# Performance work log

Measured on AMD Instinct MI355X. Metric: run time of the kernel, lower is better.

Reference implementation:

```python
import jax, jax.numpy as jnp
import numpy as np
import math

N = 8192
DIM = 256

def setup_inputs() -> dict:
    key = jax.random.key(0)
    k1, k2, k3 = jax.random.split(key, 3)
    h = jax.random.normal(k1, (N, DIM), dtype=jnp.float32)
    # xavier_uniform with gain=1.414 for square [dim, dim] matrices
    gain = 1.414
    bound = gain * math.sqrt(6.0 / (DIM + DIM))
    Wq = jax.random.uniform(k2, (DIM, DIM), dtype=jnp.float32, minval=-bound, maxval=bound)
    Wk = jax.random.uniform(k3, (DIM, DIM), dtype=jnp.float32, minval=-bound, maxval=bound)
    return {"h": h, "Wq": Wq, "Wk": Wk}

def reference(h, Wq, Wk):
    dim = h.shape[1]
    q = h @ Wq                                   # [N, dim]
    k = h @ Wk                                   # [N, dim]
    e = (q @ k.T) / jnp.sqrt(jnp.asarray(dim, h.dtype))  # [N, N]
    attention = jax.nn.softmax(e, axis=1)        # row-wise softmax
    attention = attention.mean(axis=0)           # [N], column-mean over rows
    x = attention @ h                            # [dim]
    return x
```

## Files before the change

### kernel.cpp

```cpp
#include <hip/hip_runtime.h>
#include <cstdint>
#include <cstddef>


#define N_ROWS 8192
#define DIM    256

typedef __bf16 bf16x8 __attribute__((ext_vector_type(8)));
typedef unsigned short u16x8 __attribute__((ext_vector_type(8)));
typedef float f32x16 __attribute__((ext_vector_type(16)));

__device__ __forceinline__ uint16_t f2bf(float f) {
    uint32_t u = __float_as_uint(f);
    uint32_t r = (u + 0x7fffu + ((u >> 16) & 1u)) >> 16;
    return (uint16_t)r;
}

__global__ __launch_bounds__(256) void proj_kernel(
        const float* __restrict__ h, const float* __restrict__ Wq,
        const float* __restrict__ Wk, uint16_t* __restrict__ qf,
        uint16_t* __restrict__ kf, float* __restrict__ l_arr,
        float* __restrict__ c_arr, float* __restrict__ out) {
    __shared__ alignas(16) uint16_t wb[256 * 128];
    __shared__ alignas(16) uint16_t rep[4][2048];
    const int tid = threadIdx.x, lane = tid & 63, wave = tid >> 6;
    const int which = blockIdx.x & 1;
    const int rt = blockIdx.x >> 1;

    if (blockIdx.x < 32)       l_arr[blockIdx.x * 256 + tid] = 0.0f;
    else if (blockIdx.x < 64)  c_arr[(blockIdx.x - 32) * 256 + tid] = 0.0f;
    else if (blockIdx.x == 64) out[tid] = 0.0f;

    const float* __restrict__ W = which ? Wk : Wq;
    uint16_t* __restrict__ dst = which ? kf : qf;
    const float scale = which ? 1.0f : 0.0625f;

    bf16x8 afrag[16];
    {
        const int r = rt * 32 + (lane & 31);
        const float* hp = h + (size_t)r * DIM + ((lane >> 5) * 8);
#pragma unroll
        for (int a0 = 0; a0 < 16; a0++) {
            float4 f0 = *(const float4*)(hp + a0 * 16);
            float4 f1 = *(const float4*)(hp + a0 * 16 + 4);
            u16x8 f;
            f[0] = f2bf(f0.x); f[1] = f2bf(f0.y); f[2] = f2bf(f0.z); f[3] = f2bf(f0.w);
            f[4] = f2bf(f1.x); f[5] = f2bf(f1.y); f[6] = f2bf(f1.z); f[7] = f2bf(f1.w);
            afrag[a0] = __builtin_bit_cast(bf16x8, f);
        }
    }

    for (int p = 0; p < 2; p++) {
        __syncthreads();
#pragma unroll
        for (int c = 0; c < 32; c++) {
            int f = c * 256 + tid;
            int k = f >> 5, nc = (f & 31) * 4;
            float4 w4 = *(const float4*)&W[(size_t)k * DIM + p * 128 + nc];
            ushort4 b;
            b.x = f2bf(w4.x); b.y = f2bf(w4.y); b.z = f2bf(w4.z); b.w = f2bf(w4.w);
            *(ushort4*)&wb[k * 128 + nc] = b;
        }
        __syncthreads();

        f32x16 acc;
#pragma unroll
        for (int i = 0; i < 16; i++) acc[i] = 0.0f;
        const int cl = wave * 32 + (lane & 31);
#pragma unroll
        for (int a0 = 0; a0 < 16; a0++) {
            const int kb = a0 * 16 + (lane >> 5) * 8;
            u16x8 f;
#pragma unroll
            for (int j = 0; j < 8; j++) f[j] = wb[(kb + j) * 128 + cl];
            acc = __builtin_amdgcn_mfma_f32_32x32x16_bf16(
                afrag[a0], __builtin_bit_cast(bf16x8, f), acc, 0, 0, 0);
        }

        {
            const int dcl = lane & 31;
            const int a0o = dcl >> 4, hi = (dcl >> 3) & 1, j = dcl & 7;
            const int ilb = 4 * (lane >> 5);
#pragma unroll
            for (int reg = 0; reg < 16; reg++) {
                int il = ilb + (reg & 3) + 8 * (reg >> 2);
                rep[wave][(size_t)((a0o * 64) + il + 32 * hi) * 8 + j] =
                    f2bf(acc[reg] * scale);
            }
            const uint4* rp = (const uint4*)&rep[wave][0];
            uint4* gp = (uint4*)(dst + (size_t)rt * 8192 +
                                 (size_t)(p * 8 + wave * 2) * 512);
            gp[lane * 2]     = rp[lane * 2];
            gp[lane * 2 + 1] = rp[lane * 2 + 1];
        }
    }
}

template <int MODE>
__global__ __launch_bounds__(256, 2) void qk_pass(
        const uint16_t* __restrict__ qf, const uint16_t* __restrict__ kf,
        float* __restrict__ l_arr, float* __restrict__ c_arr) {
    __shared__ float c_lds[512];
    const int tid = threadIdx.x, lane = tid & 63, wave = tid >> 6;
    const int bid = blockIdx.x;
    const int cc = ((bid & 7) << 1) | ((bid >> 3) & 1);
    const int rb = bid >> 4;
    const int t0 = rb * 8 + wave * 2;

    const uint4* qp = (const uint4*)qf;
    bf16x8 q0[16], q1[16];
#pragma unroll
    for (int a0 = 0; a0 < 16; a0++) {
        q0[a0] = __builtin_bit_cast(bf16x8, qp[(size_t)t0 * 1024 + a0 * 64 + lane]);
        q1[a0] = __builtin_bit_cast(bf16x8, qp[(size_t)(t0 + 1) * 1024 + a0 * 64 + lane]);
    }

    float rs0[16], rs1[16];
    float rr0[16], rr1[16];
    if (MODE == 0) {
#pragma unroll
        for (int r = 0; r < 16; r++) { rs0[r] = 0.0f; rs1[r] = 0.0f; }
    } else {
#pragma unroll
        for (int r = 0; r < 16; r++) {
            int ro = (r & 3) + 8 * (r >> 2) + 4 * (lane >> 5);
            rr0[r] = 1.0f / (8192.0f * l_arr[t0 * 32 + ro]);
            rr1[r] = 1.0f / (8192.0f * l_arr[(t0 + 1) * 32 + ro]);
        }
        for (int i = tid; i < 512; i += 256) c_lds[i] = 0.0f;
        __syncthreads();
    }

    const uint4* kp = (const uint4*)kf;
    bf16x8 b[2][4];
    {
        const uint4* kt = kp + (size_t)(cc * 16) * 1024;
#pragma unroll
        for (int i = 0; i < 4; i++)
            b[0][i] = __builtin_bit_cast(bf16x8, kt[i * 64 + lane]);
    }

    f32x16 acc0, acc1;
#pragma unroll
    for (int i = 0; i < 16; i++) { acc0[i] = 0.0f; acc1[i] = 0.0f; }

    for (int s = 0; s < 16; s++) {
        const uint4* kt  = kp + (size_t)(cc * 16 + s) * 1024;
        const uint4* ktn = kt + 1024;
#pragma unroll
        for (int qd = 0; qd < 4; qd++) {
            const int cur = qd & 1, nxt = cur ^ 1;
            if (qd < 3) {
#pragma unroll
                for (int i = 0; i < 4; i++)
                    b[nxt][i] = __builtin_bit_cast(bf16x8,
                        kt[((qd + 1) * 4 + i) * 64 + lane]);
            } else if (s < 15) {
#pragma unroll
                for (int i = 0; i < 4; i++)
                    b[nxt][i] = __builtin_bit_cast(bf16x8, ktn[i * 64 + lane]);
            }
#pragma unroll
            for (int i = 0; i < 4; i++) {
                acc0 = __builtin_amdgcn_mfma_f32_32x32x16_bf16(
                    q0[qd * 4 + i], b[cur][i], acc0, 0, 0, 0);
                acc1 = __builtin_amdgcn_mfma_f32_32x32x16_bf16(
                    q1[qd * 4 + i], b[cur][i], acc1, 0, 0, 0);
            }
        }
        if (MODE == 0) {
#pragma unroll
            for (int r = 0; r < 16; r++) {
                rs0[r] += __expf(acc0[r]);  acc0[r] = 0.0f;
                rs1[r] += __expf(acc1[r]);  acc1[r] = 0.0f;
            }
        } else {
            float sv = 0.0f;
#pragma unroll
            for (int r = 0; r < 16; r++) {
                sv += __expf(acc0[r]) * rr0[r];  acc0[r] = 0.0f;
                sv += __expf(acc1[r]) * rr1[r];  acc1[r] = 0.0f;
            }
            sv += __shfl_xor(sv, 32);
            if (lane < 32) atomicAdd(&c_lds[s * 32 + lane], sv);
        }
    }

    if (MODE == 0) {
#pragma unroll
        for (int r = 0; r < 16; r++) {
            int ro = (r & 3) + 8 * (r >> 2) + 4 * (lane >> 5);
            float v0 = rs0[r], v1 = rs1[r];
            v0 += __shfl_xor(v0, 1);  v0 += __shfl_xor(v0, 2);
            v0 += __shfl_xor(v0, 4);  v0 += __shfl_xor(v0, 8);
            v0 += __shfl_xor(v0, 16);
            v1 += __shfl_xor(v1, 1);  v1 += __shfl_xor(v1, 2);
            v1 += __shfl_xor(v1, 4);  v1 += __shfl_xor(v1, 8);
            v1 += __shfl_xor(v1, 16);
            if ((lane & 31) == 0) {
                atomicAdd(&l_arr[t0 * 32 + ro], v0);
                atomicAdd(&l_arr[(t0 + 1) * 32 + ro], v1);
            }
        }
    } else {
        __syncthreads();
        for (int i = tid; i < 512; i += 256) atomicAdd(&c_arr[cc * 512 + i], c_lds[i]);
    }
}

__global__ __launch_bounds__(256) void finish_kernel(
        const float* __restrict__ h, const float* __restrict__ c_arr,
        float* __restrict__ out) {
    const int d = threadIdx.x;
    const int j0 = blockIdx.x * 64;
    float acc = 0.0f;
    for (int j = j0; j < j0 + 64; j++) acc += c_arr[j] * h[(size_t)j * DIM + d];
    atomicAdd(&out[d], acc);
}

extern "C" void kernel_launch(void* const* d_in, const int* in_sizes, int n_in,
                              void* d_out, int out_size, void* d_ws, size_t ws_size,
                              hipStream_t stream) {
    const float* h  = (const float*)d_in[0];
    const float* Wq = (const float*)d_in[1];
    const float* Wk = (const float*)d_in[2];

    uint16_t* qf = (uint16_t*)d_ws;
    uint16_t* kf = qf + (size_t)N_ROWS * DIM;
    float* l_arr = (float*)((char*)d_ws + (size_t)8 * 1024 * 1024);
    float* c_arr = l_arr + N_ROWS;
    float* out = (float*)d_out;

    proj_kernel<<<512, 256, 0, stream>>>(h, Wq, Wk, qf, kf, l_arr, c_arr, out);
    qk_pass<0><<<512, 256, 0, stream>>>(qf, kf, l_arr, c_arr);
    qk_pass<1><<<512, 256, 0, stream>>>(qf, kf, l_arr, c_arr);
    finish_kernel<<<128, 256, 0, stream>>>(h, c_arr, out);
}
```

Before: 182.1 us.

## Retile QK passes per XCD, split accumulators, use exp2, stage h via LDS

The QK passes are retiled so each wave handles one 32-row Q tile across 32 K column tiles, with block-to-XCD mapping chosen for L2 locality. Two interleaved MFMA accumulators break the dependency chain. The log2(e) factor is folded into the Q scale so the native exp2 can be used. Occupancy hint rises to 3 blocks per CU, and the projection kernel now stages h through LDS, reusing the weight buffer for output repacking. The trade-off is reloading K tiles per single Q tile, which halves K reuse per MFMA compared with the previous two-tile scheme.

```diff
diff --git a/kernel.cpp b/kernel.cpp
--- a/kernel.cpp
+++ b/kernel.cpp
@@ -14,6 +14,14 @@
     uint32_t u = __float_as_uint(f);
     uint32_t r = (u + 0x7fffu + ((u >> 16) & 1u)) >> 16;
     return (uint16_t)r;
+}
+
+__device__ __forceinline__ float fexp2(float x) {
+#if __has_builtin(__builtin_amdgcn_exp2f)
+    return __builtin_amdgcn_exp2f(x);
+#else
+    return __expf(x * 0.69314718056f);
+#endif
 }
 
 __global__ __launch_bounds__(256) void proj_kernel(
@@ -22,7 +30,6 @@
         uint16_t* __restrict__ kf, float* __restrict__ l_arr,
         float* __restrict__ c_arr, float* __restrict__ out) {
     __shared__ alignas(16) uint16_t wb[256 * 128];
-    __shared__ alignas(16) uint16_t rep[4][2048];
     const int tid = threadIdx.x, lane = tid & 63, wave = tid >> 6;
     const int which = blockIdx.x & 1;
     const int rt = blockIdx.x >> 1;
@@ -33,16 +40,27 @@
 
     const float* __restrict__ W = which ? Wk : Wq;
     uint16_t* __restrict__ dst = which ? kf : qf;
-    const float scale = which ? 1.0f : 0.0625f;
+    const float scale = which ? 1.0f : (0.0625f * 1.44269504089f);
+
+    {
+        float* hb = (float*)wb;
+        for (int i = tid; i < 2048; i += 256) {
+            int r = i >> 6, c = (i & 63) * 4;
+            float4 v = *(const float4*)&h[(size_t)(rt * 32 + r) * DIM + c];
+            *(float4*)&hb[r * 260 + c] = v;
+        }
+    }
+    __syncthreads();
 
     bf16x8 afrag[16];
     {
-        const int r = rt * 32 + (lane & 31);
-        const float* hp = h + (size_t)r * DIM + ((lane >> 5) * 8);
+        const float* hb = (const float*)wb;
+        const int r = lane & 31;
 #pragma unroll
         for (int a0 = 0; a0 < 16; a0++) {
-            float4 f0 = *(const float4*)(hp + a0 * 16);
-            float4 f1 = *(const float4*)(hp + a0 * 16 + 4);
+            const int c0 = a0 * 16 + (lane >> 5) * 8;
+            float4 f0 = *(const float4*)&hb[r * 260 + c0];
+            float4 f1 = *(const float4*)&hb[r * 260 + c0 + 4];
             u16x8 f;
             f[0] = f2bf(f0.x); f[1] = f2bf(f0.y); f[2] = f2bf(f0.z); f[3] = f2bf(f0.w);
             f[4] = f2bf(f1.x); f[5] = f2bf(f1.y); f[6] = f2bf(f1.z); f[7] = f2bf(f1.w);
@@ -76,76 +94,78 @@
             acc = __builtin_amdgcn_mfma_f32_32x32x16_bf16(
                 afrag[a0], __builtin_bit_cast(bf16x8, f), acc, 0, 0, 0);
         }
+        __syncthreads();
 
         {
+            uint16_t* rp = &wb[wave * 2048];
             const int dcl = lane & 31;
             const int a0o = dcl >> 4, hi = (dcl >> 3) & 1, j = dcl & 7;
             const int ilb = 4 * (lane >> 5);
 #pragma unroll
             for (int reg = 0; reg < 16; reg++) {
                 int il = ilb + (reg & 3) + 8 * (reg >> 2);
-                rep[wave][(size_t)((a0o * 64) + il + 32 * hi) * 8 + j] =
+                rp[(size_t)((a0o * 64) + il + 32 * hi) * 8 + j] =
                     f2bf(acc[reg] * scale);
             }
-            const uint4* rp = (const uint4*)&rep[wave][0];
+            const uint4* rv = (const uint4*)rp;
             uint4* gp = (uint4*)(dst + (size_t)rt * 8192 +
                                  (size_t)(p * 8 + wave * 2) * 512);
-            gp[lane * 2]     = rp[lane * 2];
-            gp[lane * 2 + 1] = rp[lane * 2 + 1];
+            gp[lane * 2]     = rv[lane * 2];
+            gp[lane * 2 + 1] = rv[lane * 2 + 1];
         }
     }
 }
 
 template <int MODE>
-__global__ __launch_bounds__(256, 2) void qk_pass(
+__global__ __launch_bounds__(256, 3) void qk_pass(
         const uint16_t* __restrict__ qf, const uint16_t* __restrict__ kf,
         float* __restrict__ l_arr, float* __restrict__ c_arr) {
-    __shared__ float c_lds[512];
+    __shared__ float c_lds[1024];
     const int tid = threadIdx.x, lane = tid & 63, wave = tid >> 6;
     const int bid = blockIdx.x;
-    const int cc = ((bid & 7) << 1) | ((bid >> 3) & 1);
-    const int rb = bid >> 4;
-    const int t0 = rb * 8 + wave * 2;
+    const int xcd = bid & 7, w = bid >> 3;
+    const int xr = xcd >> 1, xc = xcd & 1;
+    const int rw = w & 15, cw = w >> 4;
+    const int t0  = xr * 64 + rw * 4 + wave;
+    const int ct0 = xc * 128 + cw * 32;
+    const int row0 = t0 * 32;
 
     const uint4* qp = (const uint4*)qf;
-    bf16x8 q0[16], q1[16];
-#pragma unroll
-    for (int a0 = 0; a0 < 16; a0++) {
-        q0[a0] = __builtin_bit_cast(bf16x8, qp[(size_t)t0 * 1024 + a0 * 64 + lane]);
-        q1[a0] = __builtin_bit_cast(bf16x8, qp[(size_t)(t0 + 1) * 1024 + a0 * 64 + lane]);
-    }
-
-    float rs0[16], rs1[16];
-    float rr0[16], rr1[16];
+    bf16x8 q[16];
+#pragma unroll
+    for (int a0 = 0; a0 < 16; a0++)
+        q[a0] = __builtin_bit_cast(bf16x8, qp[(size_t)t0 * 1024 + a0 * 64 + lane]);
+
+    float rs[16];
+    float rr[16];
     if (MODE == 0) {
 #pragma unroll
-        for (int r = 0; r < 16; r++) { rs0[r] = 0.0f; rs1[r] = 0.0f; }
+        for (int r = 0; r < 16; r++) rs[r] = 0.0f;
     } else {
 #pragma unroll
         for (int r = 0; r < 16; r++) {
             int ro = (r & 3) + 8 * (r >> 2) + 4 * (lane >> 5);
-            rr0[r] = 1.0f / (8192.0f * l_arr[t0 * 32 + ro]);
-            rr1[r] = 1.0f / (8192.0f * l_arr[(t0 + 1) * 32 + ro]);
-        }
-        for (int i = tid; i < 512; i += 256) c_lds[i] = 0.0f;
+            rr[r] = 1.0f / (8192.0f * l_arr[row0 + ro]);
+        }
+        for (int i = tid; i < 1024; i += 256) c_lds[i] = 0.0f;
         __syncthreads();
     }
 
     const uint4* kp = (const uint4*)kf;
     bf16x8 b[2][4];
     {
-        const uint4* kt = kp + (size_t)(cc * 16) * 1024;
+        const uint4* kt = kp + (size_t)ct0 * 1024;
 #pragma unroll
         for (int i = 0; i < 4; i++)
             b[0][i] = __builtin_bit_cast(bf16x8, kt[i * 64 + lane]);
     }
 
-    f32x16 acc0, acc1;
-#pragma unroll
-    for (int i = 0; i < 16; i++) { acc0[i] = 0.0f; acc1[i] = 0.0f; }
-
-    for (int s = 0; s < 16; s++) {
-        const uint4* kt  = kp + (size_t)(cc * 16 + s) * 1024;
+    f32x16 ae, ao;
+#pragma unroll
+    for (int i = 0; i < 16; i++) { ae[i] = 0.0f; ao[i] = 0.0f; }
+
+    for (int t = 0; t < 32; t++) {
+        const uint4* kt  = kp + (size_t)(ct0 + t) * 1024;
         const uint4* ktn = kt + 1024;
 #pragma unroll
         for (int qd = 0; qd < 4; qd++) {
@@ -155,56 +175,49 @@
                 for (int i = 0; i < 4; i++)
                     b[nxt][i] = __builtin_bit_cast(bf16x8,
                         kt[((qd + 1) * 4 + i) * 64 + lane]);
-            } else if (s < 15) {
+            } else if (t < 31) {
 #pragma unroll
                 for (int i = 0; i < 4; i++)
                     b[nxt][i] = __builtin_bit_cast(bf16x8, ktn[i * 64 + lane]);
             }
-#pragma unroll
-            for (int i = 0; i < 4; i++) {
-                acc0 = __builtin_amdgcn_mfma_f32_32x32x16_bf16(
-                    q0[qd * 4 + i], b[cur][i], acc0, 0, 0, 0);
-                acc1 = __builtin_amdgcn_mfma_f32_32x32x16_bf16(
-                    q1[qd * 4 + i], b[cur][i], acc1, 0, 0, 0);
-            }
+            ae = __builtin_amdgcn_mfma_f32_32x32x16_bf16(q[qd * 4 + 0], b[cur][0], ae, 0, 0, 0);
+            ao = __builtin_amdgcn_mfma_f32_32x32x16_bf16(q[qd * 4 + 1], b[cur][1], ao, 0, 0, 0);
+            ae = __builtin_amdgcn_mfma_f32_32x32x16_bf16(q[qd * 4 + 2], b[cur][2], ae, 0, 0, 0);
+            ao = __builtin_amdgcn_mfma_f32_32x32x16_bf16(q[qd * 4 + 3], b[cur][3], ao, 0, 0, 0);
         }
         if (MODE == 0) {
 #pragma unroll
             for (int r = 0; r < 16; r++) {
-                rs0[r] += __expf(acc0[r]);  acc0[r] = 0.0f;
-                rs1[r] += __expf(acc1[r]);  acc1[r] = 0.0f;
+                rs[r] += fexp2(ae[r] + ao[r]);
+                ae[r] = 0.0f;  ao[r] = 0.0f;
             }
         } else {
             float sv = 0.0f;
 #pragma unroll
             for (int r = 0; r < 16; r++) {
-                sv += __expf(acc0[r]) * rr0[r];  acc0[r] = 0.0f;
-                sv += __expf(acc1[r]) * rr1[r];  acc1[r] = 0.0f;
+                sv += fexp2(ae[r] + ao[r]) * rr[r];
+                ae[r] = 0.0f;  ao[r] = 0.0f;
             }
             sv += __shfl_xor(sv, 32);
-            if (lane < 32) atomicAdd(&c_lds[s * 32 + lane], sv);
+            if (lane < 32) atomicAdd(&c_lds[t * 32 + lane], sv);
         }
     }
 
     if (MODE == 0) {
 #pragma unroll
         for (int r = 0; r < 16; r++) {
-            int ro = (r & 3) + 8 * (r >> 2) + 4 * (lane >> 5);
-            float v0 = rs0[r], v1 = rs1[r];
-            v0 += __shfl_xor(v0, 1);  v0 += __shfl_xor(v0, 2);
-            v0 += __shfl_xor(v0, 4);  v0 += __shfl_xor(v0, 8);
-            v0 += __shfl_xor(v0, 16);
-            v1 += __shfl_xor(v1, 1);  v1 += __shfl_xor(v1, 2);
-            v1 += __shfl_xor(v1, 4);  v1 += __shfl_xor(v1, 8);
-            v1 += __shfl_xor(v1, 16);
+            float v = rs[r];
+            v += __shfl_xor(v, 1);  v += __shfl_xor(v, 2);  v += __shfl_xor(v, 4);
+            v += __shfl_xor(v, 8);  v += __shfl_xor(v, 16);
             if ((lane & 31) == 0) {
-                atomicAdd(&l_arr[t0 * 32 + ro], v0);
-                atomicAdd(&l_arr[(t0 + 1) * 32 + ro], v1);
+                int ro = (r & 3) + 8 * (r >> 2) + 4 * (lane >> 5);
+                atomicAdd(&l_arr[row0 + ro], v);
             }
         }
     } else {
         __syncthreads();
-        for (int i = tid; i < 512; i += 256) atomicAdd(&c_arr[cc * 512 + i], c_lds[i]);
+        for (int i = tid; i < 1024; i += 256)
+            atomicAdd(&c_arr[ct0 * 32 + i], c_lds[i]);
     }
 }
 
```

Measured after the change: 205.2 us. 12.7% more time.
